# Kernel tuning notes

Hardware: AMD Instinct MI355X
Metric: run time of the kernel (lower is better)

## Reference

```python
import jax, jax.numpy as jnp
import numpy as np

EPS = 1e-6  # torch F.pairwise_distance default eps (added to the elementwise difference)
XI = 1.2


def _pdist(A, B):
    # dist[i, j] = || B[j] - A[i] + EPS ||_2  == || (B[j]+EPS) - A[i] ||_2
    Bp = B + EPS
    sq = (jnp.sum(Bp * Bp, axis=-1)[None, :]
          + jnp.sum(A * A, axis=-1)[:, None]
          - 2.0 * A @ Bp.T)
    return jnp.sqrt(jnp.maximum(sq, 0.0))


def _half_loss(D, M):
    # D: [B, B] distances, row i = anchor. M: [B, B] float same-label mask.
    same_max = jnp.max(D * M, axis=1)                      # max over same-label distances
    diff = D * (1.0 - M)                                   # zero at same-label slots
    diff_max = jnp.max(diff, axis=1)
    # replace same-label slots with diff_max so min picks the smallest diff-label distance
    diff_min = jnp.min(M * diff_max[:, None] + diff, axis=1)
    l = same_max - diff_min + XI
    return jnp.sum(jax.nn.relu(l))


def setup_inputs() -> dict:
    key = jax.random.key(0)
    k1, k2, k3 = jax.random.split(key, 3)
    B, d = 4096, 1024
    v_f = jax.random.normal(k1, (B, d), dtype=jnp.float32)
    i_f = jax.random.normal(k2, (B, d), dtype=jnp.float32)
    y = jax.random.randint(k3, (B,), 0, 64, dtype=jnp.int64)
    return {"v_f": v_f, "i_f": i_f, "y": y}


def reference(v_f, i_f, y):
    M = (y[:, None] == y[None, :]).astype(v_f.dtype)
    # loop 1: anchor i_f[i] vs all v_f  -> D1[i, j] = ||v_f[j] - i_f[i] + eps||
    loss_i = _half_loss(_pdist(i_f, v_f), M)
    # loop 2: anchor v_f[i] vs all i_f  -> D2[i, j] = ||i_f[j] - v_f[i] + eps||
    loss_v = _half_loss(_pdist(v_f, i_f), M)
    return loss_i + loss_v
```

## Files before the change

### kernel.cpp

```cpp
#include <hip/hip_runtime.h>
#include <hip/hip_bf16.h>
#include <hip/hip_fp8.h>


#define MDIM 4096
#define KDIM 1024
#define NT   16

typedef __attribute__((ext_vector_type(16))) float f32x16;
typedef __attribute__((ext_vector_type(8)))  int   i32x8;

__device__ __forceinline__ void gload16(const void* g, void* l) {
  __builtin_amdgcn_global_load_lds(
      (const __attribute__((address_space(1))) void*)g,
      (__attribute__((address_space(3))) void*)l,
      16, 0, 0);
}

__device__ __forceinline__ unsigned char f2e4m3(float x) {
  __hip_fp8_e4m3 q(x);
  return (unsigned char)q.__x;
}

#define BAR() do { asm volatile("" ::: "memory"); \
                   __builtin_amdgcn_s_barrier();  \
                   asm volatile("" ::: "memory"); } while (0)

__global__ __launch_bounds__(256) void prep_kernel(
    const float* __restrict__ vf, const float* __restrict__ iff,
    unsigned char* __restrict__ vb8, unsigned char* __restrict__ ib8,
    float* __restrict__ ni, float* __restrict__ nvp,
    int* __restrict__ same_sq, int* __restrict__ diff_sq,
    float* __restrict__ out) {
  const int wid = blockIdx.x * 4 + (threadIdx.x >> 6);
  const int lane = threadIdx.x & 63;
  const int mat = wid >> 12;
  const int row = wid & 4095;
  const float* X = mat ? iff : vf;
  unsigned char* Xb = mat ? ib8 : vb8;

  const float4* xr4 = (const float4*)(X + (size_t)row * KDIM);
  uchar4* xb4 = (uchar4*)(Xb + (size_t)row * KDIM);

  float s = 0.0f;
#pragma unroll
  for (int it = 0; it < 4; ++it) {
    const int idx = it * 64 + lane;
    float4 v = xr4[idx];
    if (mat) {
      s += v.x * v.x + v.y * v.y + v.z * v.z + v.w * v.w;
    } else {
      float ex = v.x + 1e-6f, ey = v.y + 1e-6f, ez = v.z + 1e-6f, ew = v.w + 1e-6f;
      s += ex * ex + ey * ey + ez * ez + ew * ew;
    }
    uchar4 o;
    o.x = f2e4m3(v.x); o.y = f2e4m3(v.y); o.z = f2e4m3(v.z); o.w = f2e4m3(v.w);
    xb4[idx] = o;
  }
  for (int off = 32; off; off >>= 1) s += __shfl_down(s, off);
  if (lane == 0) {
    if (mat) ni[row] = s; else nvp[row] = s;
  }

  const int gi = blockIdx.x * 256 + threadIdx.x;
  if (gi < 2 * MDIM) {
    same_sq[gi] = 0;
    diff_sq[gi] = 0x7F800000;
  }
  if (gi == 0) out[0] = 0.0f;
}

__global__ __launch_bounds__(512, 4) void tri_gemm(
    const unsigned char* __restrict__ vb8, const unsigned char* __restrict__ ib8,
    const float* __restrict__ ni, const float* __restrict__ nvp,
    const int* __restrict__ y,
    int* __restrict__ same_sq, int* __restrict__ diff_sq) {
  __shared__ unsigned char Abuf[2][16384];
  __shared__ unsigned char Bbuf[2][8192];
  __shared__ int   yrow[256], ycol[128];
  __shared__ float nAr[256], nBc[128];

  const int row0 = blockIdx.y * 256;
  const int col0 = blockIdx.x * 128;

  const int t = threadIdx.x;
  const int w = t >> 6, lane = t & 63;
  const int l32 = lane & 31, hi = lane >> 5;
  const int wr = w >> 1, wc = w & 1;

  const int s_ksub = (t >> 6) & 1;
  const int s_r32  = (t >> 1) & 31;
  const int s_b16  = t & 1;
  const int s_koff = s_ksub * 32 + s_b16 * 16;

  auto stageA = [&](unsigned char (&buf)[16384], int h, int k0s) {
    const int g = h * 4 + (t >> 7);
    const unsigned char* src =
        ib8 + (size_t)(row0 + g * 32 + s_r32) * KDIM + k0s + s_koff;
    gload16(src, &buf[h * 8192 + (w << 10)]);
  };
  auto stageB = [&](unsigned char (&buf)[8192], int k0s) {
    const int g = t >> 7;
    const unsigned char* src =
        vb8 + (size_t)(col0 + g * 32 + s_r32) * KDIM + k0s + s_koff;
    gload16(src, &buf[w << 10]);
  };
  auto ldA = [&](const unsigned char (&buf)[16384], int R) -> i32x8 {
    return *(const i32x8*)&buf[(2 * wr + R) * 2048 + lane * 32];
  };
  auto ldB = [&](const unsigned char (&buf)[8192], int Cb) -> i32x8 {
    return *(const i32x8*)&buf[(wc * 2 + Cb) * 2048 + lane * 32];
  };

  stageA(Abuf[0], 0, 0);
  stageA(Abuf[0], 1, 0);
  stageB(Bbuf[0], 0);
  stageA(Abuf[1], 0, 64);
  stageA(Abuf[1], 1, 64);
  stageB(Bbuf[1], 64);
  if (t < 256) {
    yrow[t] = y[row0 + t];
    nAr[t] = ni[row0 + t];
  } else if (t < 384) {
    const int c = t - 256;
    ycol[c] = y[col0 + c];
    nBc[c] = nvp[col0 + c];
  }
  asm volatile("s_waitcnt vmcnt(3) lgkmcnt(0)" ::: "memory");
  BAR();

  f32x16 acc[2][2] = {};
  i32x8 aF0, aF1, bFa, bFb;

#define DO_TILE(C, K2)                                                         \
  do {                                                                         \
    aF0 = ldA(Abuf[C], 0);                                                     \
    aF1 = ldA(Abuf[C], 1);                                                     \
    bFa = ldB(Bbuf[C], 0);                                                     \
    bFb = ldB(Bbuf[C], 1);                                                     \
    BAR();                                                                     \
    stageA(Abuf[C], 0, (K2));                                                  \
    stageA(Abuf[C], 1, (K2));                                                  \
    stageB(Bbuf[C], (K2));                                                     \
    __builtin_amdgcn_s_setprio(1);                                             \
    acc[0][0] = __builtin_amdgcn_mfma_scale_f32_32x32x64_f8f6f4(               \
        aF0, bFa, acc[0][0], 0, 0, 0, 0x7F7F7F7F, 0, 0x7F7F7F7F);              \
    acc[1][0] = __builtin_amdgcn_mfma_scale_f32_32x32x64_f8f6f4(               \
        aF1, bFa, acc[1][0], 0, 0, 0, 0x7F7F7F7F, 0, 0x7F7F7F7F);              \
    acc[0][1] = __builtin_amdgcn_mfma_scale_f32_32x32x64_f8f6f4(               \
        aF0, bFb, acc[0][1], 0, 0, 0, 0x7F7F7F7F, 0, 0x7F7F7F7F);              \
    acc[1][1] = __builtin_amdgcn_mfma_scale_f32_32x32x64_f8f6f4(               \
        aF1, bFb, acc[1][1], 0, 0, 0, 0x7F7F7F7F, 0, 0x7F7F7F7F);              \
    __builtin_amdgcn_s_setprio(0);                                             \
    asm volatile("s_waitcnt vmcnt(3)" ::: "memory");                           \
    BAR();                                                                     \
  } while (0)

  for (int kt = 0; kt < NT; kt += 2) {
    const int kb = ((kt + 2) & (NT - 1)) * 64;
    const int kc = ((kt + 3) & (NT - 1)) * 64;
    DO_TILE(0, kb);
    DO_TILE(1, kc);
  }
#undef DO_TILE
  asm volatile("s_waitcnt vmcnt(0)" ::: "memory");

  const int rbase0 = row0;
  const int rbase1 = MDIM + col0;
  const float INF = __int_as_float(0x7F800000);

  float cs[2] = {0.0f, 0.0f};
  float cd[2] = {INF, INF};

#pragma unroll
  for (int R = 0; R < 2; ++R) {
#pragma unroll
    for (int g = 0; g < 16; ++g) {
      const int row_loc = wr * 64 + R * 32 + (g & 3) + 8 * (g >> 2) + 4 * hi;
      const float na = nAr[row_loc];
      const int yl = yrow[row_loc];
      float smax = 0.0f;
      float dmin = INF;
#pragma unroll
      for (int Cb = 0; Cb < 2; ++Cb) {
        const int col_loc = wc * 64 + Cb * 32 + l32;
        const float sq = fmaxf(na + nBc[col_loc] - 2.0f * acc[R][Cb][g], 0.0f);
        if (ycol[col_loc] == yl) {
          smax = fmaxf(smax, sq);
          cs[Cb] = fmaxf(cs[Cb], sq);
        } else {
          dmin = fminf(dmin, sq);
          cd[Cb] = fminf(cd[Cb], sq);
        }
      }
#pragma unroll
      for (int off = 1; off < 32; off <<= 1) {
        smax = fmaxf(smax, __shfl_xor(smax, off));
        dmin = fminf(dmin, __shfl_xor(dmin, off));
      }
      if (l32 == g) {
        atomicMax(&same_sq[rbase0 + row_loc], __float_as_int(smax));
        atomicMin(&diff_sq[rbase0 + row_loc], __float_as_int(dmin));
      }
    }
  }
#pragma unroll
  for (int Cb = 0; Cb < 2; ++Cb) {
    float s = cs[Cb], d = cd[Cb];
    s = fmaxf(s, __shfl_xor(s, 32));
    d = fminf(d, __shfl_xor(d, 32));
    if (hi == 0) {
      const int col_loc = wc * 64 + Cb * 32 + l32;
      atomicMax(&same_sq[rbase1 + col_loc], __float_as_int(s));
      atomicMin(&diff_sq[rbase1 + col_loc], __float_as_int(d));
    }
  }
}

__global__ __launch_bounds__(256) void finalize_kernel(
    const int* __restrict__ same_sq, const int* __restrict__ diff_sq,
    float* __restrict__ out) {
  const int i = blockIdx.x * 256 + threadIdx.x;
  const float sm = sqrtf(__int_as_float(same_sq[i]));
  const float dm = sqrtf(__int_as_float(diff_sq[i]));
  float l = fmaxf(sm - dm + 1.2f, 0.0f);
  for (int off = 32; off; off >>= 1) l += __shfl_down(l, off);
  __shared__ float part[4];
  const int w = threadIdx.x >> 6, lane = threadIdx.x & 63;
  if (lane == 0) part[w] = l;
  __syncthreads();
  if (threadIdx.x == 0) atomicAdd(out, part[0] + part[1] + part[2] + part[3]);
}

extern "C" void kernel_launch(void* const* d_in, const int* in_sizes, int n_in,
                              void* d_out, int out_size, void* d_ws, size_t ws_size,
                              hipStream_t stream) {
  const float* vf = (const float*)d_in[0];
  const float* iff = (const float*)d_in[1];
  const int* y = (const int*)d_in[2];
  float* out = (float*)d_out;

  char* ws = (char*)d_ws;
  unsigned char* vb8 = (unsigned char*)ws;
  unsigned char* ib8 = (unsigned char*)(ws + (4u << 20));
  float* nv  = (float*)(ws + (8u << 20));
  float* ni  = nv + 4096;
  float* nvp = nv + 2 * 4096;
  int* same_sq = (int*)(nv + 4 * 4096);
  int* diff_sq = same_sq + 2 * 4096;

  prep_kernel<<<2048, 256, 0, stream>>>(vf, iff, vb8, ib8, ni, nvp,
                                        same_sq, diff_sq, out);
  tri_gemm<<<dim3(32, 16), 512, 0, stream>>>(vb8, ib8, ni, nvp, y,
                                             same_sq, diff_sq);
  finalize_kernel<<<32, 256, 0, stream>>>(same_sq, diff_sq, out);
}
```

Before: 63.97 us.

## Shrink GEMM tile to 128x128 with 256 threads and reorganize LDS staging layout

The fused distance GEMM tile drops from 256x128 with 8 waves to 128x128 with 4 waves, doubling the grid to 1024 blocks. A shared staging lambda replaces the separate A and B loaders, and the LDS layout changes so each MFMA fragment is read as two 16-byte loads instead of one 32-byte load. The wait counts are adjusted to the new number of in-flight loads. The aim is more blocks for better CU occupancy and load balance and possibly fewer LDS bank conflicts, at the cost of lower operand reuse per block and more global traffic.

```diff
diff --git a/kernel.cpp b/kernel.cpp
--- a/kernel.cpp
+++ b/kernel.cpp
@@ -9,6 +9,7 @@
 
 typedef __attribute__((ext_vector_type(16))) float f32x16;
 typedef __attribute__((ext_vector_type(8)))  int   i32x8;
+typedef __attribute__((ext_vector_type(4)))  int   i32x4;
 
 __device__ __forceinline__ void gload16(const void* g, void* l) {
   __builtin_amdgcn_global_load_lds(
@@ -70,17 +71,17 @@
   if (gi == 0) out[0] = 0.0f;
 }
 
-__global__ __launch_bounds__(512, 4) void tri_gemm(
+__global__ __launch_bounds__(256, 4) void tri_gemm(
     const unsigned char* __restrict__ vb8, const unsigned char* __restrict__ ib8,
     const float* __restrict__ ni, const float* __restrict__ nvp,
     const int* __restrict__ y,
     int* __restrict__ same_sq, int* __restrict__ diff_sq) {
-  __shared__ unsigned char Abuf[2][16384];
+  __shared__ unsigned char Abuf[2][8192];
   __shared__ unsigned char Bbuf[2][8192];
-  __shared__ int   yrow[256], ycol[128];
-  __shared__ float nAr[256], nBc[128];
-
-  const int row0 = blockIdx.y * 256;
+  __shared__ int   yrow[128], ycol[128];
+  __shared__ float nAr[128], nBc[128];
+
+  const int row0 = blockIdx.y * 128;
   const int col0 = blockIdx.x * 128;
 
   const int t = threadIdx.x;
@@ -88,45 +89,43 @@
   const int l32 = lane & 31, hi = lane >> 5;
   const int wr = w >> 1, wc = w & 1;
 
-  const int s_ksub = (t >> 6) & 1;
-  const int s_r32  = (t >> 1) & 31;
-  const int s_b16  = t & 1;
-  const int s_koff = s_ksub * 32 + s_b16 * 16;
-
-  auto stageA = [&](unsigned char (&buf)[16384], int h, int k0s) {
-    const int g = h * 4 + (t >> 7);
+  const int s_g_lo = t >> 7;
+  const int s_row32 = t & 31;
+  const int s_koff = ((t >> 5) & 1) * 32 + ((t >> 6) & 1) * 16;
+
+  auto stage = [&](const unsigned char* __restrict__ X, int base,
+                   unsigned char (&buf)[8192], int u, int k0s) {
+    const int g = u * 2 + s_g_lo;
     const unsigned char* src =
-        ib8 + (size_t)(row0 + g * 32 + s_r32) * KDIM + k0s + s_koff;
-    gload16(src, &buf[h * 8192 + (w << 10)]);
+        X + (size_t)(base + g * 32 + s_row32) * KDIM + k0s + s_koff;
+    gload16(src, &buf[u * 4096 + (w << 10)]);
   };
-  auto stageB = [&](unsigned char (&buf)[8192], int k0s) {
-    const int g = t >> 7;
-    const unsigned char* src =
-        vb8 + (size_t)(col0 + g * 32 + s_r32) * KDIM + k0s + s_koff;
-    gload16(src, &buf[w << 10]);
+  auto ldfrag = [&](const unsigned char (&buf)[8192], int g) -> i32x8 {
+    const i32x4 lo = *(const i32x4*)&buf[g * 2048 + lane * 16];
+    const i32x4 hi4 = *(const i32x4*)&buf[g * 2048 + 1024 + lane * 16];
+    i32x8 r;
+    r[0] = lo[0]; r[1] = lo[1]; r[2] = lo[2]; r[3] = lo[3];
+    r[4] = hi4[0]; r[5] = hi4[1]; r[6] = hi4[2]; r[7] = hi4[3];
+    return r;
   };
-  auto ldA = [&](const unsigned char (&buf)[16384], int R) -> i32x8 {
-    return *(const i32x8*)&buf[(2 * wr + R) * 2048 + lane * 32];
-  };
-  auto ldB = [&](const unsigned char (&buf)[8192], int Cb) -> i32x8 {
-    return *(const i32x8*)&buf[(wc * 2 + Cb) * 2048 + lane * 32];
-  };
-
-  stageA(Abuf[0], 0, 0);
-  stageA(Abuf[0], 1, 0);
-  stageB(Bbuf[0], 0);
-  stageA(Abuf[1], 0, 64);
-  stageA(Abuf[1], 1, 64);
-  stageB(Bbuf[1], 64);
-  if (t < 256) {
+
+  stage(ib8, row0, Abuf[0], 0, 0);
+  stage(ib8, row0, Abuf[0], 1, 0);
+  stage(vb8, col0, Bbuf[0], 0, 0);
+  stage(vb8, col0, Bbuf[0], 1, 0);
+  stage(ib8, row0, Abuf[1], 0, 64);
+  stage(ib8, row0, Abuf[1], 1, 64);
+  stage(vb8, col0, Bbuf[1], 0, 64);
+  stage(vb8, col0, Bbuf[1], 1, 64);
+  if (t < 128) {
     yrow[t] = y[row0 + t];
     nAr[t] = ni[row0 + t];
-  } else if (t < 384) {
-    const int c = t - 256;
+  } else {
+    const int c = t - 128;
     ycol[c] = y[col0 + c];
     nBc[c] = nvp[col0 + c];
   }
-  asm volatile("s_waitcnt vmcnt(3) lgkmcnt(0)" ::: "memory");
+  asm volatile("s_waitcnt vmcnt(4) lgkmcnt(0)" ::: "memory");
   BAR();
 
   f32x16 acc[2][2] = {};
@@ -134,14 +133,15 @@
 
 #define DO_TILE(C, K2)                                                         \
   do {                                                                         \
-    aF0 = ldA(Abuf[C], 0);                                                     \
-    aF1 = ldA(Abuf[C], 1);                                                     \
-    bFa = ldB(Bbuf[C], 0);                                                     \
-    bFb = ldB(Bbuf[C], 1);                                                     \
+    aF0 = ldfrag(Abuf[C], wr * 2 + 0);                                         \
+    aF1 = ldfrag(Abuf[C], wr * 2 + 1);                                         \
+    bFa = ldfrag(Bbuf[C], wc * 2 + 0);                                         \
+    bFb = ldfrag(Bbuf[C], wc * 2 + 1);                                         \
     BAR();                                                                     \
-    stageA(Abuf[C], 0, (K2));                                                  \
-    stageA(Abuf[C], 1, (K2));                                                  \
-    stageB(Bbuf[C], (K2));                                                     \
+    stage(ib8, row0, Abuf[C], 0, (K2));                                        \
+    stage(ib8, row0, Abuf[C], 1, (K2));                                        \
+    stage(vb8, col0, Bbuf[C], 0, (K2));                                        \
+    stage(vb8, col0, Bbuf[C], 1, (K2));                                        \
     __builtin_amdgcn_s_setprio(1);                                             \
     acc[0][0] = __builtin_amdgcn_mfma_scale_f32_32x32x64_f8f6f4(               \
         aF0, bFa, acc[0][0], 0, 0, 0, 0x7F7F7F7F, 0, 0x7F7F7F7F);              \
@@ -152,7 +152,7 @@
     acc[1][1] = __builtin_amdgcn_mfma_scale_f32_32x32x64_f8f6f4(               \
         aF1, bFb, acc[1][1], 0, 0, 0, 0x7F7F7F7F, 0, 0x7F7F7F7F);              \
     __builtin_amdgcn_s_setprio(0);                                             \
-    asm volatile("s_waitcnt vmcnt(3)" ::: "memory");                           \
+    asm volatile("s_waitcnt vmcnt(4)" ::: "memory");                           \
     BAR();                                                                     \
   } while (0)
 
@@ -251,7 +251,7 @@
 
   prep_kernel<<<2048, 256, 0, stream>>>(vf, iff, vb8, ib8, ni, nvp,
                                         same_sq, diff_sq, out);
-  tri_gemm<<<dim3(32, 16), 512, 0, stream>>>(vb8, ib8, ni, nvp, y,
+  tri_gemm<<<dim3(32, 32), 256, 0, stream>>>(vb8, ib8, ni, nvp, y,
                                              same_sq, diff_sq);
   finalize_kernel<<<32, 256, 0, stream>>>(same_sq, diff_sq, out);
 }
```

After: 91.61 us. +43.2%, slower.
